# Performance work log

Hardware: AMD Instinct MI355X
Metric: run time of the kernel (lower is better)

Reference implementation:

```python
import jax, jax.numpy as jnp
import numpy as np

HEADS = 4
DIM_HEAD = 32
DIM = 128
EPS = 1e-5


def layer_norm(x, g, b):
    m = jnp.mean(x, axis=-1, keepdims=True)
    v = jnp.var(x, axis=-1, keepdims=True)
    return (x - m) * jax.lax.rsqrt(v + EPS) * g + b


def setup_inputs() -> dict:
    key = jax.random.key(0)
    ks = jax.random.split(key, 24)
    B, D, Hb, Wb = 1, DIM, 50, 50
    N, h, w = 6, 24, 44
    Q = Hb * Wb
    NK = N * h * w
    inner = HEADS * DIM_HEAD
    s = 0.02
    inp = {
        'q': jax.random.normal(ks[0], (B, D, Hb, Wb), jnp.float32),
        'k': jax.random.normal(ks[1], (B, N, D, h, w), jnp.float32),
        'v': jax.random.normal(ks[2], (B, N, D, h, w), jnp.float32),
        'W_logits': jax.random.uniform(ks[3], (B, Q, NK), jnp.float32),
        'vis': jax.random.randint(ks[4], (B, Q, NK), 0, 2, jnp.int32),
        'skip': jax.random.normal(ks[5], (B, D, Hb, Wb), jnp.float32),
        'qn_g': jnp.ones((D,)), 'qn_b': jnp.zeros((D,)),
        'kn_g': jnp.ones((D,)), 'kn_b': jnp.zeros((D,)),
        'vn_g': jnp.ones((D,)), 'vn_b': jnp.zeros((D,)),
        'wq': s * jax.random.normal(ks[6], (inner, D)), 'bq': jnp.zeros((inner,)),
        'wk': s * jax.random.normal(ks[7], (inner, D)), 'bk': jnp.zeros((inner,)),
        'wv': s * jax.random.normal(ks[8], (inner, D)), 'bv': jnp.zeros((inner,)),
        'wproj': s * jax.random.normal(ks[9], (D, inner)), 'bproj': jnp.zeros((D,)),
        'pre_g': jnp.ones((D,)), 'pre_b': jnp.zeros((D,)),
        'w1': s * jax.random.normal(ks[10], (2 * D, D)), 'b1': jnp.zeros((2 * D,)),
        'w2': s * jax.random.normal(ks[11], (D, 2 * D)), 'b2': jnp.zeros((D,)),
        'post_g': jnp.ones((D,)), 'post_b': jnp.zeros((D,)),
    }
    return inp


def reference(q, k, v, W_logits, vis, skip,
              qn_g, qn_b, kn_g, kn_b, vn_g, vn_b,
              wq, bq, wk, bk, wv, bv, wproj, bproj,
              pre_g, pre_b, w1, b1, w2, b2, post_g, post_b):
    B, D, Hb, Wb = q.shape
    Q = Hb * Wb
    scale = DIM_HEAD ** (-0.5)
    # flatten: q -> [B, Q, D]; k,v [B,N,D,h,w] -> [B, NK, D]
    qf = q.reshape(B, D, Q).transpose(0, 2, 1)
    kf = jnp.transpose(k, (0, 1, 3, 4, 2)).reshape(B, -1, D)
    vf = jnp.transpose(v, (0, 1, 3, 4, 2)).reshape(B, -1, D)
    qf = layer_norm(qf, qn_g, qn_b) @ wq.T + bq
    kf = layer_norm(kf, kn_g, kn_b) @ wk.T + bk
    vf = layer_norm(vf, vn_g, vn_b) @ wv.T + bv
    # split heads -> [B, H, Q/K, dh]
    qh = qf.reshape(B, Q, HEADS, DIM_HEAD).transpose(0, 2, 1, 3)
    kh = kf.reshape(B, -1, HEADS, DIM_HEAD).transpose(0, 2, 1, 3)
    vh = vf.reshape(B, -1, HEADS, DIM_HEAD).transpose(0, 2, 1, 3)
    logits = jnp.einsum('bhqd,bhkd->bhqk', qh, kh) * scale
    neg_inf = jnp.finfo(logits.dtype).min
    logits = jnp.where(vis[:, None] == 0, neg_inf, logits)
    logits = logits * W_logits[:, None]
    attn = jax.nn.softmax(logits, axis=-1)
    out = jnp.einsum('bhqk,bhkd->bhqd', attn, vh)
    out = out.transpose(0, 2, 1, 3).reshape(B, Q, HEADS * DIM_HEAD)
    out = out @ wproj.T + bproj
    z = out.transpose(0, 2, 1).reshape(B, D, Hb, Wb) + skip
    zf = z.reshape(B, D, Q).transpose(0, 2, 1)
    zf = layer_norm(zf, pre_g, pre_b)
    hmid = jax.nn.gelu(zf @ w1.T + b1, approximate=False)
    zf = zf + (hmid @ w2.T + b2)
    zf = layer_norm(zf, post_g, post_b)
    return zf.transpose(0, 2, 1).reshape(B, D, Hb, Wb)
```

## Files before the change

### kernel.cpp

```cpp
#include <hip/hip_runtime.h>
#include <hip/hip_bf16.h>

typedef __attribute__((ext_vector_type(8))) short bf16x8;
typedef __attribute__((ext_vector_type(4))) float f32x4;

#define NQ 2500
#define NKK 6336
#define NHEADS 4
#define DHEAD 32
#define CSC 0.25503482f
#define BIGNEG (-1.0e30f)

#define WS_QP 0
#define WS_KP 640000
#define WS_VT 2262016
#define WS_WB 3884032
#define WS_OP 4146176
#define OSPLIT_F 340000
#define OROW_F 136
#define WS_REQ3 8226176ULL

#define WQB 0
#define WKB 16384
#define WVB 32768
#define WPROJB 49152
#define W1B 65536
#define W2B 98304

#define NTILES_TOTAL 99
#define TQ 16
#define ATQ 32
#define TK 64
#define QBLOCKS 157
#define AQBLOCKS 79

#define PSTR 72
#define QSTR 36

__device__ __forceinline__ unsigned short bf16bits(float x) {
  union { __hip_bfloat16 h; unsigned short s; } cv;
  cv.h = __float2bfloat16(x);
  return cv.s;
}

__device__ __forceinline__ unsigned short fastbf16(float x) {
  union { float f; unsigned int u; } c; c.f = x;
  unsigned int r = c.u + 0x7fffu + ((c.u >> 16) & 1u);
  return (unsigned short)(r >> 16);
}

__global__ __launch_bounds__(256) void wconv_kernel(
    const float* __restrict__ wq, const float* __restrict__ wk,
    const float* __restrict__ wv, const float* __restrict__ wproj,
    const float* __restrict__ w1, const float* __restrict__ w2,
    __hip_bfloat16* __restrict__ wb)
{
  int e = (blockIdx.x * 256 + threadIdx.x) * 4;
  const float* src; int off;
  if (e < 16384)      { src = wq;    off = e; }
  else if (e < 32768) { src = wk;    off = e - 16384; }
  else if (e < 49152) { src = wv;    off = e - 32768; }
  else if (e < 65536) { src = wproj; off = e - 49152; }
  else if (e < 98304) { src = w1;    off = e - 65536; }
  else                { src = w2;    off = e - 98304; }
  float4 v = *(const float4*)(src + off);
  ushort4 o4;
  o4.x = bf16bits(v.x); o4.y = bf16bits(v.y); o4.z = bf16bits(v.z); o4.w = bf16bits(v.w);
  *(ushort4*)((unsigned short*)wb + e) = o4;
}

__global__ __launch_bounds__(256) void lnproj_kernel(
    const float* __restrict__ qin, const float* __restrict__ kin, const float* __restrict__ vin,
    const float* __restrict__ qn_g, const float* __restrict__ qn_b,
    const float* __restrict__ kn_g, const float* __restrict__ kn_b,
    const float* __restrict__ vn_g, const float* __restrict__ vn_b,
    const __hip_bfloat16* __restrict__ wball,
    const float* __restrict__ bq, const float* __restrict__ bk, const float* __restrict__ bv,
    __hip_bfloat16* __restrict__ Qp, __hip_bfloat16* __restrict__ Kp,
    __hip_bfloat16* __restrict__ Vt)
{
  __shared__ __hip_bfloat16 lxb[32][136];
  __shared__ float lpart[32][8][2];
  __shared__ float lmr[32][2];
  __shared__ float lgb[128], lbeb[128];

  const int t = threadIdx.x;
  const int bb = blockIdx.x;
  int mode, row0;
  const float *in, *g, *be, *bo;
  const __hip_bfloat16* wb;
  if (bb < 79)       { mode = 0; row0 = bb * 32;         in = qin; g = qn_g; be = qn_b; wb = wball + WQB; bo = bq; }
  else if (bb < 277) { mode = 1; row0 = (bb - 79) * 32;  in = kin; g = kn_g; be = kn_b; wb = wball + WKB; bo = bk; }
  else               { mode = 2; row0 = (bb - 277) * 32; in = vin; g = vn_g; be = vn_b; wb = wball + WVB; bo = bv; }

  if (t < 128) { lgb[t] = g[t]; lbeb[t] = be[t]; }

  const int row = t & 31, seg = t >> 5;
  int grow = row0 + row;
  size_t base, dstr;
  bool rvalid = true;
  if (mode == 0) { rvalid = (grow < NQ); base = (size_t)(rvalid ? grow : NQ - 1); dstr = NQ; }
  else { int n = grow / 1056, rr = grow - n * 1056; base = (size_t)n * 135168 + rr; dstr = 1056; }

  float xr[16];
  float s = 0.f, ss = 0.f;
  #pragma unroll
  for (int i = 0; i < 16; ++i) {
    float x = in[base + (size_t)(seg * 16 + i) * dstr];
    xr[i] = x; s += x; ss += x * x;
  }
  lpart[row][seg][0] = s; lpart[row][seg][1] = ss;
  __syncthreads();
  if (t < 32) {
    float S = 0.f, SS = 0.f;
    #pragma unroll
    for (int j = 0; j < 8; ++j) { S += lpart[t][j][0]; SS += lpart[t][j][1]; }
    float mean = S * (1.f / 128.f);
    float var  = SS * (1.f / 128.f) - mean * mean;
    lmr[t][0] = mean;
    lmr[t][1] = rsqrtf(fmaxf(var, 0.f) + 1e-5f);
  }
  __syncthreads();
  {
    float mean = lmr[row][0], rstd = lmr[row][1];
    #pragma unroll
    for (int i = 0; i < 16; ++i) {
      int d = seg * 16 + i;
      lxb[row][d] = __float2bfloat16((xr[i] - mean) * rstd * lgb[d] + lbeb[d]);
    }
  }
  __syncthreads();

  const int wid = t >> 6, lane = t & 63;
  const int n16 = lane & 15, quad = lane >> 4;
  const int ow = wid * 32;

  f32x4 acc[2][2] = {};
  for (int kt = 0; kt < 4; ++kt) {
    bf16x8 af[2];
    #pragma unroll
    for (int mi = 0; mi < 2; ++mi)
      af[mi] = *(const bf16x8*)&lxb[mi * 16 + n16][kt * 32 + quad * 8];
    #pragma unroll
    for (int ni = 0; ni < 2; ++ni) {
      bf16x8 bw = *(const bf16x8*)(wb + (size_t)(ow + ni * 16 + n16) * 128 + kt * 32 + quad * 8);
      #pragma unroll
      for (int mi = 0; mi < 2; ++mi)
        acc[mi][ni] = __builtin_amdgcn_mfma_f32_16x16x32_bf16(af[mi], bw, acc[mi][ni], 0, 0, 0);
    }
  }

  float bias[2];
  #pragma unroll
  for (int ni = 0; ni < 2; ++ni) bias[ni] = bo[ow + ni * 16 + n16];

  #pragma unroll
  for (int mi = 0; mi < 2; ++mi) {
    int gr0 = row0 + mi * 16 + quad * 4;
    if (mode == 2) {
      #pragma unroll
      for (int ni = 0; ni < 2; ++ni) {
        int o = ow + ni * 16 + n16;
        ushort4 v4;
        v4.x = bf16bits(acc[mi][ni][0] + bias[ni]);
        v4.y = bf16bits(acc[mi][ni][1] + bias[ni]);
        v4.z = bf16bits(acc[mi][ni][2] + bias[ni]);
        v4.w = bf16bits(acc[mi][ni][3] + bias[ni]);
        *(ushort4*)((unsigned short*)Vt + (size_t)o * NKK + gr0) = v4;
      }
    } else {
      #pragma unroll
      for (int rg = 0; rg < 4; ++rg) {
        int gr = gr0 + rg;
        if (mode != 0 || gr < NQ) {
          #pragma unroll
          for (int ni = 0; ni < 2; ++ni) {
            int o = ow + ni * 16 + n16;
            __hip_bfloat16 b16 = __float2bfloat16(acc[mi][ni][rg] + bias[ni]);
            if (mode == 0) Qp[(size_t)gr * 128 + o] = b16;
            else           Kp[(size_t)gr * 128 + o] = b16;
          }
        }
      }
    }
  }
}

__global__ __launch_bounds__(256, 3) void attn_kernel(
    const __hip_bfloat16* __restrict__ Qp,
    const __hip_bfloat16* __restrict__ Kp,
    const __hip_bfloat16* __restrict__ Vt,
    const float* __restrict__ Wl,
    const int* __restrict__ vis,
    float* __restrict__ Opart)
{
  __shared__ alignas(16) float scT[2][TK * QSTR];
  __shared__ alignas(16) __hip_bfloat16 lp[NHEADS][ATQ * PSTR];

  const int t = threadIdx.x;
  const int lane = t & 63;
  const int h = t >> 6;
  const int n16 = lane & 15;
  const int quad = lane >> 4;
  const int q0 = blockIdx.x * ATQ;
  const int split = blockIdx.y;
  const int ksplit = gridDim.y;
  const int tstart = (NTILES_TOTAL * split) / ksplit;
  const int ntiles = (NTILES_TOTAL * (split + 1)) / ksplit - tstart;

  bf16x8 aq[2];
  #pragma unroll
  for (int m = 0; m < 2; ++m) {
    int gqa = q0 + m * 16 + n16; if (gqa >= NQ) gqa = NQ - 1;
    aq[m] = *(const bf16x8*)(Qp + (size_t)gqa * 128 + h * DHEAD + quad * 8);
  }

  const int qq = t >> 3, kkc = (t & 7) * 8;
  int gqe = q0 + qq; if (gqe >= NQ) gqe = NQ - 1;
  const float* wlp = Wl  + (size_t)gqe * NKK + kkc + (size_t)tstart * TK;
  const int*   vsp = vis + (size_t)gqe * NKK + kkc + (size_t)tstart * TK;

  const __hip_bfloat16* kp[4];
  #pragma unroll
  for (int ks = 0; ks < 4; ++ks)
    kp[ks] = Kp + (size_t)(tstart * TK + ks * 16 + n16) * 128 + h * DHEAD + quad * 8;
  const __hip_bfloat16* vp0 = Vt + (size_t)(h * DHEAD + n16) * NKK + tstart * TK + quad * 8;
  const __hip_bfloat16* vp1 = vp0 + (size_t)16 * NKK;

  unsigned short* lpw = (unsigned short*)&lp[h][quad * 4 * PSTR + n16];
  const unsigned short* lpr = (const unsigned short*)&lp[h][n16 * PSTR + quad * 8];
  const int swidx = kkc * QSTR + (((qq >> 2) ^ (kkc >> 3)) << 2) + (qq & 3);
  float* swA = &scT[0][swidx];
  float* swB = &scT[1][swidx];
  const float* scrA = &scT[0][n16 * QSTR];
  const float* scrB = &scT[1][n16 * QSTR];
  const int hi8 = n16 >> 3;

  bf16x8 bones;
  {
    short one = (short)0x3F80;
    short val = (n16 == 0) ? one : (short)0;
    #pragma unroll
    for (int j = 0; j < 8; ++j) bones[j] = val;
  }

  float4 pw0, pw1; int4 pvs0, pvs1;

  auto issue = [&]() {
    pw0  = *(const float4*)(wlp);
    pw1  = *(const float4*)(wlp + 4);
    pvs0 = *(const int4*)(vsp);
    pvs1 = *(const int4*)(vsp + 4);
    wlp += TK; vsp += TK;
  };
  auto commit = [&](float* swp) {
    float c[8];
    c[0] = pvs0.x ? pw0.x * CSC : BIGNEG * pw0.x;
    c[1] = pvs0.y ? pw0.y * CSC : BIGNEG * pw0.y;
    c[2] = pvs0.z ? pw0.z * CSC : BIGNEG * pw0.z;
    c[3] = pvs0.w ? pw0.w * CSC : BIGNEG * pw0.w;
    c[4] = pvs1.x ? pw1.x * CSC : BIGNEG * pw1.x;
    c[5] = pvs1.y ? pw1.y * CSC : BIGNEG * pw1.y;
    c[6] = pvs1.z ? pw1.z * CSC : BIGNEG * pw1.z;
    c[7] = pvs1.w ? pw1.w * CSC : BIGNEG * pw1.w;
    #pragma unroll
    for (int i = 0; i < 8; ++i)
      swp[i * QSTR] = c[i];
  };

  f32x4 o[2][3];
  #pragma unroll
  for (int m = 0; m < 2; ++m)
    #pragma unroll
    for (int j = 0; j < 3; ++j)
      o[m][j] = f32x4{0.f, 0.f, 0.f, 0.f};

  issue();
  commit(swA);
  __syncthreads();

  for (int kt = 0; kt < ntiles; ++kt) {
    const float* scp = (kt & 1) ? scrB : scrA;
    float* swp = (kt & 1) ? swA : swB;
    if (kt + 1 < ntiles) issue();

    f32x4 s[2][4];
    #pragma unroll
    for (int ks = 0; ks < 4; ++ks) {
      bf16x8 bk = *(const bf16x8*)kp[ks];
      kp[ks] += TK * 128;
      f32x4 z = {0.f, 0.f, 0.f, 0.f};
      s[0][ks] = __builtin_amdgcn_mfma_f32_16x16x32_bf16(aq[0], bk, z, 0, 0, 0);
      s[1][ks] = __builtin_amdgcn_mfma_f32_16x16x32_bf16(aq[1], bk, z, 0, 0, 0);
    }

    bf16x8 bv[2][2];
    #pragma unroll
    for (int kk = 0; kk < 2; ++kk) {
      bv[kk][0] = *(const bf16x8*)(vp0 + kk * 32);
      bv[kk][1] = *(const bf16x8*)(vp1 + kk * 32);
    }
    vp0 += TK; vp1 += TK;

    #pragma unroll
    for (int m = 0; m < 2; ++m) {
      #pragma unroll
      for (int ks = 0; ks < 4; ++ks) {
        int ch = (m * 4 + quad) ^ (2 * ks + hi8);
        float4 c4 = *(const float4*)(scp + ks * 16 * QSTR + ch * 4);
        #pragma unroll
        for (int r = 0; r < 4; ++r) {
          float cr = (r == 0) ? c4.x : (r == 1) ? c4.y : (r == 2) ? c4.z : c4.w;
          float tt = fminf(s[m][ks][r] * cr, 60.f);
          float arg = (cr >= 0.f) ? tt : cr;
          float p;
          asm("v_exp_f32 %0, %1" : "=v"(p) : "v"(arg));
          lpw[m * 1152 + r * 72 + ks * 16] = fastbf16(p);
        }
      }
    }

    #pragma unroll
    for (int kk = 0; kk < 2; ++kk) {
      #pragma unroll
      for (int m = 0; m < 2; ++m) {
        bf16x8 ap = *(const bf16x8*)(lpr + m * 1152 + kk * 32);
        o[m][0] = __builtin_amdgcn_mfma_f32_16x16x32_bf16(ap, bv[kk][0], o[m][0], 0, 0, 0);
        o[m][1] = __builtin_amdgcn_mfma_f32_16x16x32_bf16(ap, bv[kk][1], o[m][1], 0, 0, 0);
        o[m][2] = __builtin_amdgcn_mfma_f32_16x16x32_bf16(ap, bones, o[m][2], 0, 0, 0);
      }
    }

    if (kt + 1 < ntiles) {
      commit(swp);
      __syncthreads();
    }
  }

  #pragma unroll
  for (int m = 0; m < 2; ++m) {
    #pragma unroll
    for (int r = 0; r < 4; ++r) {
      int gq = q0 + m * 16 + quad * 4 + r;
      if (gq < NQ) {
        float* rowp = Opart + (size_t)split * OSPLIT_F + (size_t)gq * OROW_F;
        rowp[h * DHEAD + n16] = o[m][0][r];
        rowp[h * DHEAD + 16 + n16] = o[m][1][r];
        if (n16 == 0) rowp[128 + h] = o[m][2][r];
      }
    }
  }
}

__global__ __launch_bounds__(256) void mlp_kernel(
    const float* __restrict__ Opart, int ksplit,
    const float* __restrict__ skip,
    const __hip_bfloat16* __restrict__ wball,
    const float* __restrict__ bproj,
    const float* __restrict__ pre_g, const float* __restrict__ pre_b,
    const float* __restrict__ b1, const float* __restrict__ b2,
    const float* __restrict__ post_g, const float* __restrict__ post_b,
    float* __restrict__ out)
{
  __shared__ __hip_bfloat16 sab[16][136];
  __shared__ __hip_bfloat16 znb[16][136];
  __shared__ float znf[16][132];
  __shared__ __hip_bfloat16 hb[16][264];
  __shared__ float part[16][4][2];

  const __hip_bfloat16* wprojb = wball + WPROJB;
  const __hip_bfloat16* w1b    = wball + W1B;
  const __hip_bfloat16* w2b    = wball + W2B;

  const int t = threadIdx.x;
  const int q0 = blockIdx.x * TQ;

  {
    int row = t >> 4, c0 = (t & 15) * 8;
    int gq = q0 + row; int cq = gq < NQ ? gq : NQ - 1;
    int head = c0 >> 5;
    float ll = 0.f;
    float acc8[8] = {};
    for (int s = 0; s < ksplit; ++s) {
      const float* rp = Opart + (size_t)s * OSPLIT_F + (size_t)cq * OROW_F;
      ll += rp[128 + head];
      float4 a = *(const float4*)(rp + c0);
      float4 b = *(const float4*)(rp + c0 + 4);
      acc8[0] += a.x; acc8[1] += a.y; acc8[2] += a.z; acc8[3] += a.w;
      acc8[4] += b.x; acc8[5] += b.y; acc8[6] += b.z; acc8[7] += b.w;
    }
    float rll = 1.f / fmaxf(ll, 1e-30f);
    #pragma unroll
    for (int i = 0; i < 8; ++i)
      sab[row][c0 + i] = __float2bfloat16(acc8[i] * rll);
  }
  __syncthreads();

  const int wid = t >> 6, lane = t & 63;
  const int n16 = lane & 15, quad = lane >> 4;
  const int qrow0 = q0 + quad * 4;

  f32x4 acc1[2] = {};
  for (int kt = 0; kt < 4; ++kt) {
    bf16x8 af = *(const bf16x8*)&sab[n16][kt * 32 + quad * 8];
    #pragma unroll
    for (int ni = 0; ni < 2; ++ni) {
      int o = wid * 32 + ni * 16 + n16;
      bf16x8 bw = *(const bf16x8*)(wprojb + (size_t)o * 128 + kt * 32 + quad * 8);
      acc1[ni] = __builtin_amdgcn_mfma_f32_16x16x32_bf16(af, bw, acc1[ni], 0, 0, 0);
    }
  }
  float z[2][4];
  #pragma unroll
  for (int ni = 0; ni < 2; ++ni) {
    int o = wid * 32 + ni * 16 + n16;
    float bo = bproj[o];
    if (qrow0 + 3 < NQ) {
      float4 sk = *(const float4*)(skip + (size_t)o * NQ + qrow0);
      z[ni][0] = acc1[ni][0] + bo + sk.x;
      z[ni][1] = acc1[ni][1] + bo + sk.y;
      z[ni][2] = acc1[ni][2] + bo + sk.z;
      z[ni][3] = acc1[ni][3] + bo + sk.w;
    } else {
      #pragma unroll
      for (int rg = 0; rg < 4; ++rg) {
        int cq = qrow0 + rg < NQ ? qrow0 + rg : NQ - 1;
        z[ni][rg] = acc1[ni][rg] + bo + skip[(size_t)o * NQ + cq];
      }
    }
  }
  #pragma unroll
  for (int rg = 0; rg < 4; ++rg) {
    float s = z[0][rg] + z[1][rg];
    float ss = z[0][rg] * z[0][rg] + z[1][rg] * z[1][rg];
    s += __shfl_xor(s, 1);  ss += __shfl_xor(ss, 1);
    s += __shfl_xor(s, 2);  ss += __shfl_xor(ss, 2);
    s += __shfl_xor(s, 4);  ss += __shfl_xor(ss, 4);
    s += __shfl_xor(s, 8);  ss += __shfl_xor(ss, 8);
    if (n16 == 0) { part[quad * 4 + rg][wid][0] = s; part[quad * 4 + rg][wid][1] = ss; }
  }
  __syncthreads();
  #pragma unroll
  for (int rg = 0; rg < 4; ++rg) {
    int row = quad * 4 + rg;
    float S  = part[row][0][0] + part[row][1][0] + part[row][2][0] + part[row][3][0];
    float SS = part[row][0][1] + part[row][1][1] + part[row][2][1] + part[row][3][1];
    float mean = S * (1.f / 128.f);
    float var  = SS * (1.f / 128.f) - mean * mean;
    float rstd = rsqrtf(fmaxf(var, 0.f) + 1e-5f);
    #pragma unroll
    for (int ni = 0; ni < 2; ++ni) {
      int o = wid * 32 + ni * 16 + n16;
      float zn = (z[ni][rg] - mean) * rstd * pre_g[o] + pre_b[o];
      znf[row][o] = zn;
      znb[row][o] = __float2bfloat16(zn);
    }
  }
  __syncthreads();

  f32x4 acc2[4] = {};
  for (int kt = 0; kt < 4; ++kt) {
    bf16x8 af = *(const bf16x8*)&znb[n16][kt * 32 + quad * 8];
    #pragma unroll
    for (int ni = 0; ni < 4; ++ni) {
      int j = wid * 64 + ni * 16 + n16;
      bf16x8 bw = *(const bf16x8*)(w1b + (size_t)j * 128 + kt * 32 + quad * 8);
      acc2[ni] = __builtin_amdgcn_mfma_f32_16x16x32_bf16(af, bw, acc2[ni], 0, 0, 0);
    }
  }
  #pragma unroll
  for (int ni = 0; ni < 4; ++ni) {
    int j = wid * 64 + ni * 16 + n16;
    float bj = b1[j];
    #pragma unroll
    for (int rg = 0; rg < 4; ++rg) {
      float a1 = acc2[ni][rg] + bj;
      hb[quad * 4 + rg][j] = __float2bfloat16(0.5f * a1 * (1.0f + erff(a1 * 0.70710678118654752f)));
    }
  }
  __syncthreads();

  f32x4 acc3[2] = {};
  for (int kt = 0; kt < 8; ++kt) {
    bf16x8 af = *(const bf16x8*)&hb[n16][kt * 32 + quad * 8];
    #pragma unroll
    for (int ni = 0; ni < 2; ++ni) {
      int o = wid * 32 + ni * 16 + n16;
      bf16x8 bw = *(const bf16x8*)(w2b + (size_t)o * 256 + kt * 32 + quad * 8);
      acc3[ni] = __builtin_amdgcn_mfma_f32_16x16x32_bf16(af, bw, acc3[ni], 0, 0, 0);
    }
  }
  float y[2][4];
  #pragma unroll
  for (int ni = 0; ni < 2; ++ni) {
    int o = wid * 32 + ni * 16 + n16;
    float bo = b2[o];
    #pragma unroll
    for (int rg = 0; rg < 4; ++rg)
      y[ni][rg] = znf[quad * 4 + rg][o] + acc3[ni][rg] + bo;
  }
  #pragma unroll
  for (int rg = 0; rg < 4; ++rg) {
    float s = y[0][rg] + y[1][rg];
    float ss = y[0][rg] * y[0][rg] + y[1][rg] * y[1][rg];
    s += __shfl_xor(s, 1);  ss += __shfl_xor(ss, 1);
    s += __shfl_xor(s, 2);  ss += __shfl_xor(ss, 2);
    s += __shfl_xor(s, 4);  ss += __shfl_xor(ss, 4);
    s += __shfl_xor(s, 8);  ss += __shfl_xor(ss, 8);
    if (n16 == 0) { part[quad * 4 + rg][wid][0] = s; part[quad * 4 + rg][wid][1] = ss; }
  }
  __syncthreads();
  #pragma unroll
  for (int rg = 0; rg < 4; ++rg) {
    int row = quad * 4 + rg;
    float S  = part[row][0][0] + part[row][1][0] + part[row][2][0] + part[row][3][0];
    float SS = part[row][0][1] + part[row][1][1] + part[row][2][1] + part[row][3][1];
    float mean = S * (1.f / 128.f);
    float var  = SS * (1.f / 128.f) - mean * mean;
    float rstd = rsqrtf(fmaxf(var, 0.f) + 1e-5f);
    #pragma unroll
    for (int ni = 0; ni < 2; ++ni) {
      int o = wid * 32 + ni * 16 + n16;
      y[ni][rg] = (y[ni][rg] - mean) * rstd * post_g[o] + post_b[o];
    }
  }
  #pragma unroll
  for (int ni = 0; ni < 2; ++ni) {
    int o = wid * 32 + ni * 16 + n16;
    if (qrow0 + 3 < NQ) {
      *(float4*)(out + (size_t)o * NQ + qrow0) = make_float4(y[ni][0], y[ni][1], y[ni][2], y[ni][3]);
    } else {
      #pragma unroll
      for (int rg = 0; rg < 4; ++rg)
        if (qrow0 + rg < NQ) out[(size_t)o * NQ + qrow0 + rg] = y[ni][rg];
    }
  }
}

extern "C" void kernel_launch(void* const* d_in, const int* in_sizes, int n_in,
                              void* d_out, int out_size, void* d_ws, size_t ws_size,
                              hipStream_t stream) {
  if (ws_size < WS_REQ3) return;
  int ksplit = (int)((ws_size - WS_OP) / (size_t)(OSPLIT_F * 4));
  if (ksplit > 12) ksplit = 12;
  if (ksplit < 3)  ksplit = 3;

  const float* q     = (const float*)d_in[0];
  const float* k     = (const float*)d_in[1];
  const float* v     = (const float*)d_in[2];
  const float* Wl    = (const float*)d_in[3];
  const int*   vis   = (const int*)d_in[4];
  const float* skip  = (const float*)d_in[5];
  const float* qn_g  = (const float*)d_in[6];
  const float* qn_b  = (const float*)d_in[7];
  const float* kn_g  = (const float*)d_in[8];
  const float* kn_b  = (const float*)d_in[9];
  const float* vn_g  = (const float*)d_in[10];
  const float* vn_b  = (const float*)d_in[11];
  const float* wq    = (const float*)d_in[12];
  const float* bq    = (const float*)d_in[13];
  const float* wk    = (const float*)d_in[14];
  const float* bk    = (const float*)d_in[15];
  const float* wv    = (const float*)d_in[16];
  const float* bv    = (const float*)d_in[17];
  const float* wproj = (const float*)d_in[18];
  const float* bproj = (const float*)d_in[19];
  const float* pre_g = (const float*)d_in[20];
  const float* pre_b = (const float*)d_in[21];
  const float* w1    = (const float*)d_in[22];
  const float* b1    = (const float*)d_in[23];
  const float* w2    = (const float*)d_in[24];
  const float* b2    = (const float*)d_in[25];
  const float* post_g= (const float*)d_in[26];
  const float* post_b= (const float*)d_in[27];

  char* ws = (char*)d_ws;
  __hip_bfloat16* Qp = (__hip_bfloat16*)(ws + WS_QP);
  __hip_bfloat16* Kp = (__hip_bfloat16*)(ws + WS_KP);
  __hip_bfloat16* Vt = (__hip_bfloat16*)(ws + WS_VT);
  __hip_bfloat16* Wb = (__hip_bfloat16*)(ws + WS_WB);
  float* Opart = (float*)(ws + WS_OP);

  hipLaunchKernelGGL(wconv_kernel, dim3(128), dim3(256), 0, stream,
                     wq, wk, wv, wproj, w1, w2, Wb);

  hipLaunchKernelGGL(lnproj_kernel, dim3(475), dim3(256), 0, stream,
                     q, k, v, qn_g, qn_b, kn_g, kn_b, vn_g, vn_b,
                     Wb, bq, bk, bv, Qp, Kp, Vt);

  hipLaunchKernelGGL(attn_kernel, dim3(AQBLOCKS, ksplit), dim3(256), 0, stream,
                     Qp, Kp, Vt, Wl, vis, Opart);

  hipLaunchKernelGGL(mlp_kernel, dim3(QBLOCKS), dim3(256), 0, stream,
                     Opart, ksplit, skip, Wb, bproj, pre_g, pre_b,
                     b1, b2, post_g, post_b, (float*)d_out);
}
```

Measured before the change: 248.6 us.

## Double-buffer logit-weight prefetch in registers and raise attention occupancy

The attention loop is unrolled by two, with alternating A/B register sets, so the W_logits and visibility loads are issued two tiles ahead instead of one. Per-tile K/V loads and MFMAs are written out explicitly, with sched_barrier fences after each prefetch. Launch bounds go from 3 to 4 blocks per CU. The aim is to hide more of the global-memory latency on the large mask and weight stream, at the cost of more live registers under a tighter register cap, which could cause spills.

```diff
diff --git a/kernel.cpp b/kernel.cpp
--- a/kernel.cpp
+++ b/kernel.cpp
@@ -186,7 +186,7 @@
   }
 }
 
-__global__ __launch_bounds__(256, 3) void attn_kernel(
+__global__ __launch_bounds__(256, 4) void attn_kernel(
     const __hip_bfloat16* __restrict__ Qp,
     const __hip_bfloat16* __restrict__ Kp,
     const __hip_bfloat16* __restrict__ Vt,
@@ -220,10 +220,10 @@
   const float* wlp = Wl  + (size_t)gqe * NKK + kkc + (size_t)tstart * TK;
   const int*   vsp = vis + (size_t)gqe * NKK + kkc + (size_t)tstart * TK;
 
-  const __hip_bfloat16* kp[4];
-  #pragma unroll
-  for (int ks = 0; ks < 4; ++ks)
-    kp[ks] = Kp + (size_t)(tstart * TK + ks * 16 + n16) * 128 + h * DHEAD + quad * 8;
+  const __hip_bfloat16* kp0 = Kp + (size_t)(tstart * TK + n16) * 128 + h * DHEAD + quad * 8;
+  const __hip_bfloat16* kp1 = kp0 + (size_t)16 * 128;
+  const __hip_bfloat16* kp2 = kp0 + (size_t)32 * 128;
+  const __hip_bfloat16* kp3 = kp0 + (size_t)48 * 128;
   const __hip_bfloat16* vp0 = Vt + (size_t)(h * DHEAD + n16) * NKK + tstart * TK + quad * 8;
   const __hip_bfloat16* vp1 = vp0 + (size_t)16 * NKK;
 
@@ -244,28 +244,47 @@
     for (int j = 0; j < 8; ++j) bones[j] = val;
   }
 
-  float4 pw0, pw1; int4 pvs0, pvs1;
-
-  auto issue = [&]() {
-    pw0  = *(const float4*)(wlp);
-    pw1  = *(const float4*)(wlp + 4);
-    pvs0 = *(const int4*)(vsp);
-    pvs1 = *(const int4*)(vsp + 4);
+  float4 pwA0, pwA1, pwB0, pwB1; int4 pvsA0, pvsA1, pvsB0, pvsB1;
+
+  auto issueA = [&]() {
+    pwA0  = *(const float4*)(wlp);
+    pwA1  = *(const float4*)(wlp + 4);
+    pvsA0 = *(const int4*)(vsp);
+    pvsA1 = *(const int4*)(vsp + 4);
     wlp += TK; vsp += TK;
   };
-  auto commit = [&](float* swp) {
+  auto issueB = [&]() {
+    pwB0  = *(const float4*)(wlp);
+    pwB1  = *(const float4*)(wlp + 4);
+    pvsB0 = *(const int4*)(vsp);
+    pvsB1 = *(const int4*)(vsp + 4);
+    wlp += TK; vsp += TK;
+  };
+  auto commitA = [&]() {
     float c[8];
-    c[0] = pvs0.x ? pw0.x * CSC : BIGNEG * pw0.x;
-    c[1] = pvs0.y ? pw0.y * CSC : BIGNEG * pw0.y;
-    c[2] = pvs0.z ? pw0.z * CSC : BIGNEG * pw0.z;
-    c[3] = pvs0.w ? pw0.w * CSC : BIGNEG * pw0.w;
-    c[4] = pvs1.x ? pw1.x * CSC : BIGNEG * pw1.x;
-    c[5] = pvs1.y ? pw1.y * CSC : BIGNEG * pw1.y;
-    c[6] = pvs1.z ? pw1.z * CSC : BIGNEG * pw1.z;
-    c[7] = pvs1.w ? pw1.w * CSC : BIGNEG * pw1.w;
-    #pragma unroll
-    for (int i = 0; i < 8; ++i)
-      swp[i * QSTR] = c[i];
+    c[0] = pvsA0.x ? pwA0.x * CSC : BIGNEG * pwA0.x;
+    c[1] = pvsA0.y ? pwA0.y * CSC : BIGNEG * pwA0.y;
+    c[2] = pvsA0.z ? pwA0.z * CSC : BIGNEG * pwA0.z;
+    c[3] = pvsA0.w ? pwA0.w * CSC : BIGNEG * pwA0.w;
+    c[4] = pvsA1.x ? pwA1.x * CSC : BIGNEG * pwA1.x;
+    c[5] = pvsA1.y ? pwA1.y * CSC : BIGNEG * pwA1.y;
+    c[6] = pvsA1.z ? pwA1.z * CSC : BIGNEG * pwA1.z;
+    c[7] = pvsA1.w ? pwA1.w * CSC : BIGNEG * pwA1.w;
+    #pragma unroll
+    for (int i = 0; i < 8; ++i) swA[i * QSTR] = c[i];
+  };
+  auto commitB = [&]() {
+    float c[8];
+    c[0] = pvsB0.x ? pwB0.x * CSC : BIGNEG * pwB0.x;
+    c[1] = pvsB0.y ? pwB0.y * CSC : BIGNEG * pwB0.y;
+    c[2] = pvsB0.z ? pwB0.z * CSC : BIGNEG * pwB0.z;
+    c[3] = pvsB0.w ? pwB0.w * CSC : BIGNEG * pwB0.w;
+    c[4] = pvsB1.x ? pwB1.x * CSC : BIGNEG * pwB1.x;
+    c[5] = pvsB1.y ? pwB1.y * CSC : BIGNEG * pwB1.y;
+    c[6] = pvsB1.z ? pwB1.z * CSC : BIGNEG * pwB1.z;
+    c[7] = pvsB1.w ? pwB1.w * CSC : BIGNEG * pwB1.w;
+    #pragma unroll
+    for (int i = 0; i < 8; ++i) swB[i * QSTR] = c[i];
   };
 
   f32x4 o[2][3];
@@ -275,31 +294,28 @@
     for (int j = 0; j < 3; ++j)
       o[m][j] = f32x4{0.f, 0.f, 0.f, 0.f};
 
-  issue();
-  commit(swA);
-  __syncthreads();
-
-  for (int kt = 0; kt < ntiles; ++kt) {
-    const float* scp = (kt & 1) ? scrB : scrA;
-    float* swp = (kt & 1) ? swA : swB;
-    if (kt + 1 < ntiles) issue();
-
+  auto body = [&](const float* scp) {
     f32x4 s[2][4];
-    #pragma unroll
-    for (int ks = 0; ks < 4; ++ks) {
-      bf16x8 bk = *(const bf16x8*)kp[ks];
-      kp[ks] += TK * 128;
+    {
+      bf16x8 bk0 = *(const bf16x8*)kp0; kp0 += TK * 128;
+      bf16x8 bk1 = *(const bf16x8*)kp1; kp1 += TK * 128;
+      bf16x8 bk2 = *(const bf16x8*)kp2; kp2 += TK * 128;
+      bf16x8 bk3 = *(const bf16x8*)kp3; kp3 += TK * 128;
       f32x4 z = {0.f, 0.f, 0.f, 0.f};
-      s[0][ks] = __builtin_amdgcn_mfma_f32_16x16x32_bf16(aq[0], bk, z, 0, 0, 0);
-      s[1][ks] = __builtin_amdgcn_mfma_f32_16x16x32_bf16(aq[1], bk, z, 0, 0, 0);
-    }
-
-    bf16x8 bv[2][2];
-    #pragma unroll
-    for (int kk = 0; kk < 2; ++kk) {
-      bv[kk][0] = *(const bf16x8*)(vp0 + kk * 32);
-      bv[kk][1] = *(const bf16x8*)(vp1 + kk * 32);
-    }
+      s[0][0] = __builtin_amdgcn_mfma_f32_16x16x32_bf16(aq[0], bk0, z, 0, 0, 0);
+      s[1][0] = __builtin_amdgcn_mfma_f32_16x16x32_bf16(aq[1], bk0, z, 0, 0, 0);
+      s[0][1] = __builtin_amdgcn_mfma_f32_16x16x32_bf16(aq[0], bk1, z, 0, 0, 0);
+      s[1][1] = __builtin_amdgcn_mfma_f32_16x16x32_bf16(aq[1], bk1, z, 0, 0, 0);
+      s[0][2] = __builtin_amdgcn_mfma_f32_16x16x32_bf16(aq[0], bk2, z, 0, 0, 0);
+      s[1][2] = __builtin_amdgcn_mfma_f32_16x16x32_bf16(aq[1], bk2, z, 0, 0, 0);
+      s[0][3] = __builtin_amdgcn_mfma_f32_16x16x32_bf16(aq[0], bk3, z, 0, 0, 0);
+      s[1][3] = __builtin_amdgcn_mfma_f32_16x16x32_bf16(aq[1], bk3, z, 0, 0, 0);
+    }
+
+    bf16x8 bv00 = *(const bf16x8*)(vp0);
+    bf16x8 bv01 = *(const bf16x8*)(vp1);
+    bf16x8 bv10 = *(const bf16x8*)(vp0 + 32);
+    bf16x8 bv11 = *(const bf16x8*)(vp1 + 32);
     vp0 += TK; vp1 += TK;
 
     #pragma unroll
@@ -320,21 +336,44 @@
       }
     }
 
-    #pragma unroll
-    for (int kk = 0; kk < 2; ++kk) {
-      #pragma unroll
-      for (int m = 0; m < 2; ++m) {
-        bf16x8 ap = *(const bf16x8*)(lpr + m * 1152 + kk * 32);
-        o[m][0] = __builtin_amdgcn_mfma_f32_16x16x32_bf16(ap, bv[kk][0], o[m][0], 0, 0, 0);
-        o[m][1] = __builtin_amdgcn_mfma_f32_16x16x32_bf16(ap, bv[kk][1], o[m][1], 0, 0, 0);
-        o[m][2] = __builtin_amdgcn_mfma_f32_16x16x32_bf16(ap, bones, o[m][2], 0, 0, 0);
-      }
-    }
-
-    if (kt + 1 < ntiles) {
-      commit(swp);
-      __syncthreads();
-    }
+    {
+      bf16x8 ap0 = *(const bf16x8*)(lpr);
+      bf16x8 ap1 = *(const bf16x8*)(lpr + 1152);
+      o[0][0] = __builtin_amdgcn_mfma_f32_16x16x32_bf16(ap0, bv00, o[0][0], 0, 0, 0);
+      o[0][1] = __builtin_amdgcn_mfma_f32_16x16x32_bf16(ap0, bv01, o[0][1], 0, 0, 0);
+      o[0][2] = __builtin_amdgcn_mfma_f32_16x16x32_bf16(ap0, bones, o[0][2], 0, 0, 0);
+      o[1][0] = __builtin_amdgcn_mfma_f32_16x16x32_bf16(ap1, bv00, o[1][0], 0, 0, 0);
+      o[1][1] = __builtin_amdgcn_mfma_f32_16x16x32_bf16(ap1, bv01, o[1][1], 0, 0, 0);
+      o[1][2] = __builtin_amdgcn_mfma_f32_16x16x32_bf16(ap1, bones, o[1][2], 0, 0, 0);
+      bf16x8 aq0 = *(const bf16x8*)(lpr + 32);
+      bf16x8 aq1 = *(const bf16x8*)(lpr + 1152 + 32);
+      o[0][0] = __builtin_amdgcn_mfma_f32_16x16x32_bf16(aq0, bv10, o[0][0], 0, 0, 0);
+      o[0][1] = __builtin_amdgcn_mfma_f32_16x16x32_bf16(aq0, bv11, o[0][1], 0, 0, 0);
+      o[0][2] = __builtin_amdgcn_mfma_f32_16x16x32_bf16(aq0, bones, o[0][2], 0, 0, 0);
+      o[1][0] = __builtin_amdgcn_mfma_f32_16x16x32_bf16(aq1, bv10, o[1][0], 0, 0, 0);
+      o[1][1] = __builtin_amdgcn_mfma_f32_16x16x32_bf16(aq1, bv11, o[1][1], 0, 0, 0);
+      o[1][2] = __builtin_amdgcn_mfma_f32_16x16x32_bf16(aq1, bones, o[1][2], 0, 0, 0);
+    }
+  };
+
+  issueA();
+  if (ntiles > 1) issueB();
+  commitA();
+  __syncthreads();
+
+  int kt = 0;
+  for (;;) {
+    if (kt + 2 < ntiles) issueA();
+    __builtin_amdgcn_sched_barrier(0);
+    body(scrA);
+    if (kt + 1 < ntiles) { commitB(); __syncthreads(); }
+    if (++kt >= ntiles) break;
+
+    if (kt + 2 < ntiles) issueB();
+    __builtin_amdgcn_sched_barrier(0);
+    body(scrB);
+    if (kt + 1 < ntiles) { commitA(); __syncthreads(); }
+    if (++kt >= ntiles) break;
   }
 
   #pragma unroll
```

Result: slower. 279.9 us (+12.6%).
